# Kernel tuning notes

Measured on AMD Instinct MI355X. Metric: run time of the kernel, lower is better.

Reference implementation:

```python
import jax, jax.numpy as jnp
import numpy as np

B, D_IN, D_OUT, H, E, K = 16384, 1024, 1024, 2048, 8, 2

def setup_inputs() -> dict:
    key = jax.random.key(0)
    ks = jax.random.split(key, 7)
    s_in = 1.0 / np.sqrt(D_IN)
    s_h = 1.0 / np.sqrt(H)
    return {
        "x": jax.random.normal(ks[0], (B, D_IN), dtype=jnp.float32),
        "router_W": jax.random.uniform(ks[1], (E, D_IN), jnp.float32, -s_in, s_in),
        "router_b": jax.random.uniform(ks[2], (E,), jnp.float32, -s_in, s_in),
        "W1": jax.random.uniform(ks[3], (E, H, D_IN), jnp.float32, -s_in, s_in),
        "b1": jax.random.uniform(ks[4], (E, H), jnp.float32, -s_in, s_in),
        "W2": jax.random.uniform(ks[5], (E, D_OUT, H), jnp.float32, -s_h, s_h),
        "b2": jax.random.uniform(ks[6], (E, D_OUT), jnp.float32, -s_h, s_h),
    }

def reference(x, router_W, router_b, W1, b1, W2, b2):
    # Router: softmax over experts, top-k selection, renormalize
    logits = x @ router_W.T + router_b                      # [B, E]
    router_probs = jax.nn.softmax(logits, axis=-1)          # [B, E]
    top_v, top_i = jax.lax.top_k(router_probs, K)           # [B, K]
    top_v = top_v / jnp.sum(top_v, axis=-1, keepdims=True)  # renormalized
    # Scatter top-k weights into dense [B, E] combine weights (zero elsewhere)
    b_idx = jnp.arange(x.shape[0])[:, None]
    combine = jnp.zeros_like(router_probs).at[b_idx, top_i].add(top_v)  # [B, E]
    # Dense per-expert MLP, combined with zero weights for unselected experts
    # (identical math to the original mask/gather/scatter loop)
    h = jax.nn.relu(jnp.einsum('bi,ehi->beh', x, W1) + b1)  # [B, E, H]
    y = jnp.einsum('beh,eoh->beo', h, W2) + b2              # [B, E, O]
    out = jnp.einsum('beo,be->bo', y, combine)              # [B, O]
    return out, router_probs
```

## Files before the change

### kernel.cpp

```cpp
#include <hip/hip_runtime.h>
#include <hip/hip_bf16.h>

#define Bsz  16384
#define Din  1024
#define Dout 1024
#define Hdim 2048
#define Ecnt 8
#define CNT_PAD 32

typedef _Float16 f16;
typedef _Float16 f16x8 __attribute__((ext_vector_type(8)));
typedef _Float16 f16x4 __attribute__((ext_vector_type(4)));
typedef float    f32x4 __attribute__((ext_vector_type(4)));

#define AS_GLOBAL __attribute__((address_space(1)))
#define AS_LDS    __attribute__((address_space(3)))

__device__ __forceinline__ void async_copy16(const void* gptr, void* lptr) {
    __builtin_amdgcn_global_load_lds(
        (const AS_GLOBAL unsigned int*)gptr,
        (AS_LDS unsigned int*)lptr, 16, 0, 0);
}

__global__ __launch_bounds__(256) void cast_kernel(
    const float* __restrict__ in, f16* __restrict__ out)
{
    int i = (blockIdx.x * 256 + threadIdx.x) * 4;
    float4 v = *(const float4*)(in + i);
    f16x4 o;
    o.x = (f16)v.x; o.y = (f16)v.y; o.z = (f16)v.z; o.w = (f16)v.w;
    *(f16x4*)(out + i) = o;
}

__global__ __launch_bounds__(256) void router_kernel(
    const float* __restrict__ x, const float* __restrict__ rW,
    const float* __restrict__ rb, float* __restrict__ probs_out,
    int* __restrict__ cnt, int* __restrict__ bucket, float* __restrict__ gates)
{
    __shared__ float s_rw[Ecnt * Din];
    __shared__ int   s_e[64];
    __shared__ float s_g[64];
    __shared__ int   s_lpos[64];
    __shared__ int   s_lcnt[Ecnt];
    __shared__ int   s_base[Ecnt];

    int t = threadIdx.x;
    if (t < Ecnt) s_lcnt[t] = 0;
    for (int i = t; i < Ecnt * Din; i += 256) s_rw[i] = rW[i];
    __syncthreads();

    int wid = t >> 6, lane = t & 63;

    float rbv[8];
    #pragma unroll
    for (int e = 0; e < 8; e++) rbv[e] = rb[e];

    #pragma unroll 2
    for (int tt = 0; tt < 8; tt++) {
        int li = wid * 8 + tt;
        int token = blockIdx.x * 32 + li;
        const float* xrow = x + (size_t)token * Din;

        float acc[8] = {0,0,0,0,0,0,0,0};
        #pragma unroll
        for (int i = 0; i < 4; i++) {
            float4 xv = *(const float4*)(xrow + i * 256 + lane * 4);
            #pragma unroll
            for (int e = 0; e < 8; e++) {
                float4 wv = *(const float4*)(s_rw + e * Din + i * 256 + lane * 4);
                acc[e] += xv.x * wv.x + xv.y * wv.y + xv.z * wv.z + xv.w * wv.w;
            }
        }
        #pragma unroll
        for (int e = 0; e < 8; e++) {
            #pragma unroll
            for (int m = 1; m < 64; m <<= 1) acc[e] += __shfl_xor(acc[e], m, 64);
        }

        float p[8], mx = -1e30f;
        #pragma unroll
        for (int e = 0; e < 8; e++) { p[e] = acc[e] + rbv[e]; mx = fmaxf(mx, p[e]); }
        float s = 0.f;
        #pragma unroll
        for (int e = 0; e < 8; e++) { p[e] = expf(p[e] - mx); s += p[e]; }
        float inv = 1.f / s;
        #pragma unroll
        for (int e = 0; e < 8; e++) p[e] *= inv;

        if (lane == 0) {
            float* po = probs_out + (size_t)token * Ecnt;
            #pragma unroll
            for (int e = 0; e < 8; e++) po[e] = p[e];
            int i0 = 0; float v0 = p[0];
            #pragma unroll
            for (int e = 1; e < 8; e++) if (p[e] > v0) { v0 = p[e]; i0 = e; }
            int i1 = -1; float v1 = -1e30f;
            #pragma unroll
            for (int e = 0; e < 8; e++) if (e != i0 && p[e] > v1) { v1 = p[e]; i1 = e; }
            float invs = 1.f / (v0 + v1);
            s_e[2 * li]     = i0;  s_g[2 * li]     = v0 * invs;
            s_e[2 * li + 1] = i1;  s_g[2 * li + 1] = v1 * invs;
        }
    }
    __syncthreads();

    if (t < 64) s_lpos[t] = atomicAdd(&s_lcnt[s_e[t]], 1);
    __syncthreads();
    if (t < Ecnt) s_base[t] = atomicAdd(&cnt[t * CNT_PAD], s_lcnt[t]);
    __syncthreads();
    if (t < 64) {
        int e = s_e[t];
        int pos = s_base[e] + s_lpos[t];
        int li = t >> 1;
        int token = blockIdx.x * 32 + li;
        bucket[e * Bsz + pos] = token * 2 + (t & 1);
        gates [e * Bsz + pos] = s_g[t];
    }
}

template<int Kd, bool G1>
__global__ __launch_bounds__(256) void moe_gemm(
    const f16* __restrict__ A, const f16* __restrict__ Wt,
    const float* __restrict__ bias, const int* __restrict__ cnt,
    const int* __restrict__ bucket, const float* __restrict__ gates,
    f16* __restrict__ hbuf, float* __restrict__ out, int Ndim)
{
    int e   = (int)blockIdx.x & 7;
    int idx = (int)blockIdx.x >> 3;
    int nx  = Ndim >> 7;
    int by  = idx / nx;
    int bx  = idx - by * nx;

    int count = min(cnt[e * CNT_PAD], Bsz);
    int m0 = by * 128;
    if (m0 >= count) return;
    int n0 = bx * 128;

    __shared__ alignas(16) f16 As[2][128 * 32];
    __shared__ alignas(16) f16 Bs[2][128 * 32];
    __shared__ int   s_rows[128];
    __shared__ float s_gates[128];

    int t = threadIdx.x;
    if (t < 128) {
        int pos = min(m0 + t, count - 1);
        s_rows[t] = bucket[e * Bsz + pos];
        if constexpr (!G1) s_gates[t] = gates[e * Bsz + pos];
    }
    __syncthreads();

    int wave = t >> 6, lane = t & 63;
    int scol = (lane & 3) * 8;

    const f16* agp[2];
    const f16* bgp[2];
    #pragma unroll
    for (int j = 0; j < 2; j++) {
        int srow = wave * 32 + j * 16 + (lane >> 2);
        int r = s_rows[srow];
        size_t arow = G1 ? (size_t)(r >> 1) : (size_t)r;
        agp[j] = A + arow * Kd + scol;
        bgp[j] = Wt + ((size_t)e * Ndim + (n0 + srow)) * (size_t)Kd + scol;
    }

    int m_w = (wave >> 1) * 64;
    int n_w = (wave & 1) * 64;
    int frow = lane & 15;
    int fk   = (lane >> 4) * 8;

    f32x4 acc[4][4] = {};

    #pragma unroll
    for (int j = 0; j < 2; j++) {
        async_copy16(agp[j], &As[0][(wave * 32 + j * 16) * 32]);
        async_copy16(bgp[j], &Bs[0][(wave * 32 + j * 16) * 32]);
        agp[j] += 32; bgp[j] += 32;
    }
    __syncthreads();

    int cur = 0;
    for (int k0 = 0; k0 < Kd; k0 += 32) {
        f16x8 af[4], bfr[4];
        #pragma unroll
        for (int i = 0; i < 4; i++) {
            af[i]  = *(const f16x8*)(&As[cur][(m_w + i * 16 + frow) * 32 + fk]);
            bfr[i] = *(const f16x8*)(&Bs[cur][(n_w + i * 16 + frow) * 32 + fk]);
        }
        if (k0 + 32 < Kd) {
            #pragma unroll
            for (int j = 0; j < 2; j++) {
                async_copy16(agp[j], &As[cur ^ 1][(wave * 32 + j * 16) * 32]);
                async_copy16(bgp[j], &Bs[cur ^ 1][(wave * 32 + j * 16) * 32]);
                agp[j] += 32; bgp[j] += 32;
            }
        }
        __builtin_amdgcn_s_setprio(1);
        #pragma unroll
        for (int i = 0; i < 4; i++)
            #pragma unroll
            for (int jj = 0; jj < 4; jj++)
                acc[i][jj] = __builtin_amdgcn_mfma_f32_16x16x32_f16(
                    af[i], bfr[jj], acc[i][jj], 0, 0, 0);
        __builtin_amdgcn_s_setprio(0);
        __syncthreads();
        cur ^= 1;
    }

    float bv[4];
    #pragma unroll
    for (int jj = 0; jj < 4; jj++)
        bv[jj] = bias[e * Ndim + n0 + n_w + jj * 16 + frow];

    #pragma unroll
    for (int i = 0; i < 4; i++) {
        int mbase = m_w + i * 16 + (lane >> 4) * 4;
        #pragma unroll
        for (int reg = 0; reg < 4; reg++) {
            int m = mbase + reg;
            if (m0 + m >= count) continue;
            int r = s_rows[m];
            if constexpr (G1) {
                f16* hrow = hbuf + (size_t)r * Hdim;
                #pragma unroll
                for (int jj = 0; jj < 4; jj++) {
                    int n = n0 + n_w + jj * 16 + frow;
                    float v = acc[i][jj][reg] + bv[jj];
                    hrow[n] = (f16)fmaxf(v, 0.f);
                }
            } else {
                int token = r >> 1;
                float g = s_gates[m];
                #pragma unroll
                for (int jj = 0; jj < 4; jj++) {
                    int n = n0 + n_w + jj * 16 + frow;
                    float v = g * (acc[i][jj][reg] + bv[jj]);
                    atomicAdd(&out[(size_t)token * Dout + n], v);
                }
            }
        }
    }
}

extern "C" void kernel_launch(void* const* d_in, const int* in_sizes, int n_in,
                              void* d_out, int out_size, void* d_ws, size_t ws_size,
                              hipStream_t stream) {
    const float* x   = (const float*)d_in[0];
    const float* rW  = (const float*)d_in[1];
    const float* rb  = (const float*)d_in[2];
    const float* W1  = (const float*)d_in[3];
    const float* b1  = (const float*)d_in[4];
    const float* W2  = (const float*)d_in[5];
    const float* b2  = (const float*)d_in[6];
    float* out   = (float*)d_out;
    float* probs = out + (size_t)Bsz * Dout;

    char* ws = (char*)d_ws;
    int*   cnt    = (int*)ws;
    int*   bucket = (int*)(ws + 0x1000);
    float* gates  = (float*)(ws + 0x90000);
    f16*   x16    = (f16*)(ws + 0x200000);
    f16*   w16    = (f16*)(ws + 0x2200000);
    f16*   hbuf   = (f16*)(ws + 0x4200000);

    hipMemsetAsync(cnt, 0, Ecnt * CNT_PAD * sizeof(int), stream);
    hipMemsetAsync(out, 0, (size_t)Bsz * Dout * sizeof(float), stream);

    cast_kernel<<<(Bsz * Din) / 1024, 256, 0, stream>>>(x, x16);
    cast_kernel<<<(Ecnt * Hdim * Din) / 1024, 256, 0, stream>>>(W1, w16);

    router_kernel<<<Bsz / 32, 256, 0, stream>>>(x, rW, rb, probs, cnt, bucket, gates);

    int nb1 = Ecnt * (Bsz / 128) * (Hdim / 128);
    moe_gemm<Din, true><<<nb1, 256, 0, stream>>>(
        x16, w16, b1, cnt, bucket, gates, hbuf, out, Hdim);

    cast_kernel<<<(Ecnt * Dout * Hdim) / 1024, 256, 0, stream>>>(W2, w16);

    int nb2 = Ecnt * (Bsz / 128) * (Dout / 128);
    moe_gemm<Hdim, false><<<nb2, 256, 0, stream>>>(
        hbuf, w16, b2, cnt, bucket, gates, hbuf, out, Dout);
}
```

Baseline: 681.6 us.

## Load weight fragments directly from global into registers, dropping LDS staging for B

The weight (B) operand is no longer staged through LDS. Each wave loads its MFMA fragments straight from global memory into registers, double-buffered in registers with the K loop unrolled by two. This frees half the LDS and removes the LDS reads for B. In exchange, the two wave pairs that share the same n columns now each fetch those weights from global, which raises L2 traffic and register pressure, and global load latency is exposed inside each step.

Result: slower. 1.020 ms (+49.7%).

```diff
diff --git a/kernel.cpp b/kernel.cpp
--- a/kernel.cpp
+++ b/kernel.cpp
@@ -137,7 +137,6 @@
     int n0 = bx * 128;
 
     __shared__ alignas(16) f16 As[2][128 * 32];
-    __shared__ alignas(16) f16 Bs[2][128 * 32];
     __shared__ int   s_rows[128];
     __shared__ float s_gates[128];
 
@@ -153,14 +152,12 @@
     int scol = (lane & 3) * 8;
 
     const f16* agp[2];
-    const f16* bgp[2];
     #pragma unroll
     for (int j = 0; j < 2; j++) {
         int srow = wave * 32 + j * 16 + (lane >> 2);
         int r = s_rows[srow];
         size_t arow = G1 ? (size_t)(r >> 1) : (size_t)r;
         agp[j] = A + arow * Kd + scol;
-        bgp[j] = Wt + ((size_t)e * Ndim + (n0 + srow)) * (size_t)Kd + scol;
     }
 
     int m_w = (wave >> 1) * 64;
@@ -168,31 +165,58 @@
     int frow = lane & 15;
     int fk   = (lane >> 4) * 8;
 
+    const f16* bp[4];
+    #pragma unroll
+    for (int jj = 0; jj < 4; jj++)
+        bp[jj] = Wt + ((size_t)e * Ndim + (n0 + n_w + jj * 16 + frow)) * (size_t)Kd + fk;
+
     f32x4 acc[4][4] = {};
+    f16x8 bA[4], bB[4];
 
     #pragma unroll
     for (int j = 0; j < 2; j++) {
         async_copy16(agp[j], &As[0][(wave * 32 + j * 16) * 32]);
-        async_copy16(bgp[j], &Bs[0][(wave * 32 + j * 16) * 32]);
-        agp[j] += 32; bgp[j] += 32;
-    }
+        agp[j] += 32;
+    }
+    #pragma unroll
+    for (int jj = 0; jj < 4; jj++) { bA[jj] = *(const f16x8*)(bp[jj]); bp[jj] += 32; }
     __syncthreads();
 
     int cur = 0;
-    for (int k0 = 0; k0 < Kd; k0 += 32) {
-        f16x8 af[4], bfr[4];
-        #pragma unroll
-        for (int i = 0; i < 4; i++) {
-            af[i]  = *(const f16x8*)(&As[cur][(m_w + i * 16 + frow) * 32 + fk]);
-            bfr[i] = *(const f16x8*)(&Bs[cur][(n_w + i * 16 + frow) * 32 + fk]);
-        }
-        if (k0 + 32 < Kd) {
+    for (int k0 = 0; k0 < Kd; k0 += 64) {
+        f16x8 af[4];
+        #pragma unroll
+        for (int i = 0; i < 4; i++)
+            af[i] = *(const f16x8*)(&As[cur][(m_w + i * 16 + frow) * 32 + fk]);
+        #pragma unroll
+        for (int j = 0; j < 2; j++) {
+            async_copy16(agp[j], &As[cur ^ 1][(wave * 32 + j * 16) * 32]);
+            agp[j] += 32;
+        }
+        #pragma unroll
+        for (int jj = 0; jj < 4; jj++) { bB[jj] = *(const f16x8*)(bp[jj]); bp[jj] += 32; }
+        __builtin_amdgcn_s_setprio(1);
+        #pragma unroll
+        for (int i = 0; i < 4; i++)
+            #pragma unroll
+            for (int jj = 0; jj < 4; jj++)
+                acc[i][jj] = __builtin_amdgcn_mfma_f32_16x16x32_f16(
+                    af[i], bA[jj], acc[i][jj], 0, 0, 0);
+        __builtin_amdgcn_s_setprio(0);
+        __syncthreads();
+        cur ^= 1;
+
+        #pragma unroll
+        for (int i = 0; i < 4; i++)
+            af[i] = *(const f16x8*)(&As[cur][(m_w + i * 16 + frow) * 32 + fk]);
+        if (k0 + 64 < Kd) {
             #pragma unroll
             for (int j = 0; j < 2; j++) {
                 async_copy16(agp[j], &As[cur ^ 1][(wave * 32 + j * 16) * 32]);
-                async_copy16(bgp[j], &Bs[cur ^ 1][(wave * 32 + j * 16) * 32]);
-                agp[j] += 32; bgp[j] += 32;
+                agp[j] += 32;
             }
+            #pragma unroll
+            for (int jj = 0; jj < 4; jj++) { bA[jj] = *(const f16x8*)(bp[jj]); bp[jj] += 32; }
         }
         __builtin_amdgcn_s_setprio(1);
         #pragma unroll
@@ -200,7 +224,7 @@
             #pragma unroll
             for (int jj = 0; jj < 4; jj++)
                 acc[i][jj] = __builtin_amdgcn_mfma_f32_16x16x32_f16(
-                    af[i], bfr[jj], acc[i][jj], 0, 0, 0);
+                    af[i], bB[jj], acc[i][jj], 0, 0, 0);
         __builtin_amdgcn_s_setprio(0);
         __syncthreads();
         cur ^= 1;
```
